# Kernel tuning notes

Measured on AMD Instinct MI355X. Metric: run time of the kernel, lower is better.

Reference implementation:

```python
import jax, jax.numpy as jnp
import numpy as np

EPS = 1e-12  # F.normalize default eps


def setup_inputs() -> dict:
    key = jax.random.key(0)
    x = jax.random.normal(key, (4, 64, 8192, 1), dtype=jnp.float32)
    return {"x": x, "k": 9, "dilation": 1}


def reference(x, k, dilation):
    # x: (B, D, N, 1)
    B, D, N, _ = x.shape
    kk = k * dilation
    # F.normalize(x, p=2, dim=1)
    norm = jnp.linalg.norm(x, axis=1, keepdims=True)
    xn = x / jnp.maximum(norm, EPS)
    # -> (B, N, D)
    pts = jnp.squeeze(xn, -1).transpose(0, 2, 1)
    # pairwise euclidean distance (cdist p=2)
    sq = jnp.sum(pts * pts, axis=-1)  # (B, N)
    d2 = sq[:, :, None] + sq[:, None, :] - 2.0 * jnp.einsum("bnd,bmd->bnm", pts, pts)
    dist = jnp.sqrt(jnp.maximum(d2, 0.0))  # (B, N, N)
    # torch.topk(-dist, k): k smallest distances
    _, nn_idx = jax.lax.top_k(-dist, kk)  # (B, N, kk)
    center_idx = jnp.broadcast_to(jnp.arange(N, dtype=nn_idx.dtype)[None, :, None], (B, N, kk))
    edge_index = jnp.stack([nn_idx, center_idx], axis=0)  # (2, B, N, kk)
    return edge_index[:, :, :, ::dilation]
```

## Files before the change

kernel.cpp:

```cpp
#include <hip/hip_runtime.h>

#define BB 4
#define DD 64
#define NN 8192
#define KK 9


typedef __attribute__((ext_vector_type(8))) _Float16 f16x8;
typedef __attribute__((ext_vector_type(16))) float f32x16;
typedef __attribute__((ext_vector_type(2))) _Float16 h2;
struct H2x4 { h2 a, b, c, d; };

__device__ __forceinline__ uint4 pack8(const unsigned* w) {
    return make_uint4(w[0] | (w[1] << 16), w[2] | (w[3] << 16),
                      w[4] | (w[5] << 16), w[6] | (w[7] << 16));
}

__device__ __forceinline__ float min3f(float a, float b, float c) {
    return fminf(fminf(a, b), c);
}

__device__ __forceinline__ float dot2acc(h2 g, h2 r, float acc) {
#if __has_builtin(__builtin_amdgcn_fdot2)
    return __builtin_amdgcn_fdot2(g, r, acc, false);
#else
    acc = fmaf((float)g[0], (float)r[0], acc);
    return fmaf((float)g[1], (float)r[1], acc);
#endif
}

__device__ __forceinline__ int s_to_j(int g, int s4) {
    int T = ((g >> 6) << 5) + (((g >> 5) & 1) << 4) + (g & 15);
    return T * 32 + ((s4 >> 2) << 3) + (((g >> 4) & 1) << 2) + (s4 & 3);
}

__global__ __launch_bounds__(256) void knorm2_kernel(const float* __restrict__ x,
                                                     float* __restrict__ xnT,
                                                     float* __restrict__ sq,
                                                     unsigned short* __restrict__ Phi,
                                                     unsigned short* __restrict__ Shi) {
    int t = blockIdx.x * 256 + threadIdx.x;
    int b = t >> 13;
    int n = t & (NN - 1);
    const float* xb = x + (size_t)b * DD * NN + n;
    float v[DD];
    float ss = 0.0f;
#pragma unroll
    for (int d = 0; d < DD; ++d) {
        v[d] = xb[(size_t)d * NN];
        ss = fmaf(v[d], v[d], ss);
    }
    float inv = 1.0f / fmaxf(sqrtf(ss), 1e-12f);
    float s2 = 0.0f;
#pragma unroll
    for (int d = 0; d < DD; ++d) {
        v[d] *= inv;
        s2 = fmaf(v[d], v[d], s2);
    }
    sq[t] = s2;
    float4* o4 = reinterpret_cast<float4*>(xnT + (size_t)t * DD);
#pragma unroll
    for (int d = 0; d < DD; d += 4) o4[d >> 2] = make_float4(v[d], v[d+1], v[d+2], v[d+3]);

    size_t base = (size_t)t * DD;
#pragma unroll
    for (int d0 = 0; d0 < DD; d0 += 8) {
        unsigned ph[8], sh[8];
#pragma unroll
        for (int e = 0; e < 8; ++e) {
            float f = v[d0 + e];
            _Float16 hp = (_Float16)f;
            _Float16 hs = (_Float16)(-2.0f * f);
            ph[e] = (unsigned)__builtin_bit_cast(unsigned short, hp);
            sh[e] = (unsigned)__builtin_bit_cast(unsigned short, hs);
        }
        *reinterpret_cast<uint4*>(Phi + base + d0) = pack8(ph);
        *reinterpret_cast<uint4*>(Shi + base + d0) = pack8(sh);
    }
}

__global__ __launch_bounds__(256, 4) void kmin_kernel(const unsigned short* __restrict__ Shi,
                                                      const unsigned short* __restrict__ Phi,
                                                      unsigned short* __restrict__ minbuf16) {
    __shared__ float stage[4][64][33];
    const int lane = threadIdx.x & 63;
    const int wave = threadIdx.x >> 6;
    const int l31 = lane & 31;
    const int half = lane >> 5;
    const int i0 = blockIdx.x * 256 + wave * 64;
    const int b = i0 >> 13;
    const int jloc0 = blockIdx.y * (NN / 8);

    f16x8 Bh0[4], Bh1[4];
    {
        const size_t ib0 = (size_t)(i0 + l31) * DD + half * 8;
        const size_t ib1 = (size_t)(i0 + 32 + l31) * DD + half * 8;
#pragma unroll
        for (int kc = 0; kc < 4; ++kc) {
            Bh0[kc] = *reinterpret_cast<const f16x8*>(Phi + ib0 + kc * 16);
            Bh1[kc] = *reinterpret_cast<const f16x8*>(Phi + ib1 + kc * 16);
        }
    }
    const size_t ja0 = ((size_t)b * NN + jloc0 + l31) * DD + half * 8;

    f16x8 A0[4], A1[4];
#pragma unroll
    for (int kc = 0; kc < 4; ++kc)
        A0[kc] = *reinterpret_cast<const f16x8*>(Shi + ja0 + kc * 16);

#pragma unroll 2
    for (int u2 = 0; u2 < 16; ++u2) {
        const int t0 = u2 * 2;
        {
            const size_t ja = ja0 + (size_t)(t0 + 1) * 32 * DD;
#pragma unroll
            for (int kc = 0; kc < 4; ++kc)
                A1[kc] = *reinterpret_cast<const f16x8*>(Shi + ja + kc * 16);
        }
        {
            f32x16 c0 = {}, c1 = {};
#pragma unroll
            for (int kc = 0; kc < 4; ++kc)
                c0 = __builtin_amdgcn_mfma_f32_32x32x16_f16(A0[kc], Bh0[kc], c0, 0, 0, 0);
#pragma unroll
            for (int kc = 0; kc < 4; ++kc)
                c1 = __builtin_amdgcn_mfma_f32_32x32x16_f16(A0[kc], Bh1[kc], c1, 0, 0, 0);
            const int col = half * 16 + (t0 & 15);
            {
                float q0 = min3f(c0[0], c0[1], c0[2]);
                float q1 = min3f(c0[3], c0[4], c0[5]);
                float q2 = min3f(c0[6], c0[7], c0[8]);
                float q3 = min3f(c0[9], c0[10], c0[11]);
                float q4 = min3f(c0[12], c0[13], c0[14]);
                stage[wave][l31][col] = fminf(min3f(q0, q1, q2), min3f(q3, q4, c0[15]));
            }
            {
                float q0 = min3f(c1[0], c1[1], c1[2]);
                float q1 = min3f(c1[3], c1[4], c1[5]);
                float q2 = min3f(c1[6], c1[7], c1[8]);
                float q3 = min3f(c1[9], c1[10], c1[11]);
                float q4 = min3f(c1[12], c1[13], c1[14]);
                stage[wave][32 + l31][col] = fminf(min3f(q0, q1, q2), min3f(q3, q4, c1[15]));
            }
        }
        if (u2 < 15) {
            const size_t ja = ja0 + (size_t)(t0 + 2) * 32 * DD;
#pragma unroll
            for (int kc = 0; kc < 4; ++kc)
                A0[kc] = *reinterpret_cast<const f16x8*>(Shi + ja + kc * 16);
        }
        {
            f32x16 c0 = {}, c1 = {};
#pragma unroll
            for (int kc = 0; kc < 4; ++kc)
                c0 = __builtin_amdgcn_mfma_f32_32x32x16_f16(A1[kc], Bh0[kc], c0, 0, 0, 0);
#pragma unroll
            for (int kc = 0; kc < 4; ++kc)
                c1 = __builtin_amdgcn_mfma_f32_32x32x16_f16(A1[kc], Bh1[kc], c1, 0, 0, 0);
            const int col = half * 16 + ((t0 + 1) & 15);
            {
                float q0 = min3f(c0[0], c0[1], c0[2]);
                float q1 = min3f(c0[3], c0[4], c0[5]);
                float q2 = min3f(c0[6], c0[7], c0[8]);
                float q3 = min3f(c0[9], c0[10], c0[11]);
                float q4 = min3f(c0[12], c0[13], c0[14]);
                stage[wave][l31][col] = fminf(min3f(q0, q1, q2), min3f(q3, q4, c0[15]));
            }
            {
                float q0 = min3f(c1[0], c1[1], c1[2]);
                float q1 = min3f(c1[3], c1[4], c1[5]);
                float q2 = min3f(c1[6], c1[7], c1[8]);
                float q3 = min3f(c1[9], c1[10], c1[11]);
                float q4 = min3f(c1[12], c1[13], c1[14]);
                stage[wave][32 + l31][col] = fminf(min3f(q0, q1, q2), min3f(q3, q4, c1[15]));
            }
        }
        if ((t0 & 15) == 14) {
            const int fph = t0 >> 4;
            unsigned short* dst0 = minbuf16 + (size_t)blockIdx.y * 64 + fph * 32;
#pragma unroll
            for (int it = 0; it < 4; ++it) {
                int idx = it * 64 + lane;
                int r = idx >> 2;
                int p = idx & 3;
                const float* s = &stage[wave][r][p * 8];
                unsigned w[8];
#pragma unroll
                for (int e = 0; e < 8; ++e)
                    w[e] = (unsigned)__builtin_bit_cast(unsigned short, (_Float16)s[e]);
                *reinterpret_cast<uint4*>(dst0 + (size_t)(i0 + r) * 512 + p * 8) = pack8(w);
            }
        }
    }
}

__global__ __launch_bounds__(256) void ksel_kernel(const float* __restrict__ xnT,
                                                   const float* __restrict__ sq,
                                                   const unsigned short* __restrict__ minbuf16,
                                                   const unsigned short* __restrict__ Phi,
                                                   int* __restrict__ out) {
    __shared__ unsigned short glist[4][2][40];
    __shared__ unsigned short jlist[4][2][64];
    const int lane = threadIdx.x & 63;
    const int wave = threadIdx.x >> 6;
    const int tA = __builtin_amdgcn_readfirstlane(blockIdx.x * 8 + wave * 2);
    const int tB = tA + 1;
    const int b = tA >> 13;
    const int nA = tA & (NN - 1);
    const int nB = tB & (NN - 1);

    float gmA[8], gmB[8];
    {
        uint4 a = *reinterpret_cast<const uint4*>(minbuf16 + (size_t)tA * 512 + lane * 8);
        uint4 c = *reinterpret_cast<const uint4*>(minbuf16 + (size_t)tB * 512 + lane * 8);
        unsigned wa[4] = {a.x, a.y, a.z, a.w};
        unsigned wb[4] = {c.x, c.y, c.z, c.w};
#pragma unroll
        for (int q4 = 0; q4 < 4; ++q4) {
            gmA[q4*2+0] = (float)__builtin_bit_cast(_Float16, (unsigned short)(wa[q4] & 0xFFFFu));
            gmA[q4*2+1] = (float)__builtin_bit_cast(_Float16, (unsigned short)(wa[q4] >> 16));
            gmB[q4*2+0] = (float)__builtin_bit_cast(_Float16, (unsigned short)(wb[q4] & 0xFFFFu));
            gmB[q4*2+1] = (float)__builtin_bit_cast(_Float16, (unsigned short)(wb[q4] >> 16));
        }
    }

    float svA = fminf(min3f(gmA[0], gmA[1], gmA[2]),
                      fminf(min3f(gmA[3], gmA[4], gmA[5]), fminf(gmA[6], gmA[7])));
    float svB = fminf(min3f(gmB[0], gmB[1], gmB[2]),
                      fminf(min3f(gmB[3], gmB[4], gmB[5]), fminf(gmB[6], gmB[7])));
#pragma unroll
    for (int k = 2; k <= 64; k <<= 1) {
#pragma unroll
        for (int jj = k >> 1; jj >= 1; jj >>= 1) {
            float oA = __shfl_xor(svA, jj);
            float oB = __shfl_xor(svB, jj);
            bool keepMin = (((lane & jj) == 0) == ((lane & k) == 0));
            svA = keepMin ? fminf(svA, oA) : fmaxf(svA, oA);
            svB = keepMin ? fminf(svB, oB) : fmaxf(svB, oB);
        }
    }
    const float th9pA = __shfl(svA, 8);
    const float th9pB = __shfl(svB, 8);
    const float thetaA  = th9pA + 8e-3f,  thetaB  = th9pB + 8e-3f;
    const float kappa1A = th9pA + 7.5e-3f, kappa1B = th9pB + 7.5e-3f;

    int cntA = 0, cntB = 0;
    unsigned short* glA = &glist[wave][0][0];
    unsigned short* glB = &glist[wave][1][0];
#pragma unroll
    for (int q = 0; q < 8; ++q) {
        bool cA = gmA[q] <= thetaA;
        unsigned long long mA = __ballot(cA);
        int pA = cntA + __popcll(mA & ((1ULL << lane) - 1ULL));
        if (cA && pA < 40) glA[pA] = (unsigned short)(lane * 8 + q);
        cntA += (int)__popcll(mA);
        bool cB = gmB[q] <= thetaB;
        unsigned long long mB = __ballot(cB);
        int pB = cntB + __popcll(mB & ((1ULL << lane) - 1ULL));
        if (cB && pB < 40) glB[pB] = (unsigned short)(lane * 8 + q);
        cntB += (int)__popcll(mB);
    }

    const unsigned short* __restrict__ Pb = Phi + ((size_t)b * NN) * DD;
    H2x4 arhA[8], arhB[8];
    {
        const f16x8* prA = reinterpret_cast<const f16x8*>(Phi + (size_t)tA * DD);
        const f16x8* prB = reinterpret_cast<const f16x8*>(Phi + (size_t)tB * DD);
#pragma unroll
        for (int c8 = 0; c8 < 8; ++c8) {
            arhA[c8] = __builtin_bit_cast(H2x4, prA[c8]);
            arhB[c8] = __builtin_bit_cast(H2x4, prB[c8]);
        }
    }

    const bool ovfA = (cntA > 40), ovfB = (cntB > 40);
    const int totalA = ovfA ? NN : cntA * 16;
    const int totalB = ovfB ? NN : cntB * 16;
    const int nItA = (totalA + 63) >> 6, nItB = (totalB + 63) >> 6;
    const int nIt = nItA > nItB ? nItA : nItB;
    int S1A = 0, S1B = 0;
    unsigned short* jlA = &jlist[wave][0][0];
    unsigned short* jlB = &jlist[wave][1][0];
#pragma unroll 1
    for (int m = 0; m < nIt; ++m) {
        const int idx = m * 64 + lane;
        const bool actA = idx < totalA;
        const bool actB = idx < totalB;
        float m2A = __uint_as_float(0x7f800000u);
        float m2B = __uint_as_float(0x7f800000u);
        int jA = 0, jB = 0;
        if (actA) {
            jA = ovfA ? idx : s_to_j((int)glA[idx >> 4], idx & 15);
            const f16x8* p8 = reinterpret_cast<const f16x8*>(Pb + (size_t)jA * DD);
            float a0 = 0.0f, a1 = 0.0f, a2 = 0.0f, a3 = 0.0f;
#pragma unroll
            for (int c8 = 0; c8 < 8; ++c8) {
                H2x4 g2 = __builtin_bit_cast(H2x4, p8[c8]);
                a0 = dot2acc(g2.a, arhA[c8].a, a0);
                a1 = dot2acc(g2.b, arhA[c8].b, a1);
                a2 = dot2acc(g2.c, arhA[c8].c, a2);
                a3 = dot2acc(g2.d, arhA[c8].d, a3);
            }
            m2A = -2.0f * ((a0 + a1) + (a2 + a3));
        }
        if (actB) {
            jB = ovfB ? idx : s_to_j((int)glB[idx >> 4], idx & 15);
            const f16x8* p8 = reinterpret_cast<const f16x8*>(Pb + (size_t)jB * DD);
            float a0 = 0.0f, a1 = 0.0f, a2 = 0.0f, a3 = 0.0f;
#pragma unroll
            for (int c8 = 0; c8 < 8; ++c8) {
                H2x4 g2 = __builtin_bit_cast(H2x4, p8[c8]);
                a0 = dot2acc(g2.a, arhB[c8].a, a0);
                a1 = dot2acc(g2.b, arhB[c8].b, a1);
                a2 = dot2acc(g2.c, arhB[c8].c, a2);
                a3 = dot2acc(g2.d, arhB[c8].d, a3);
            }
            m2B = -2.0f * ((a0 + a1) + (a2 + a3));
        }
        bool passA = actA && (m2A <= kappa1A);
        unsigned long long mA = __ballot(passA);
        int pA = S1A + __popcll(mA & ((1ULL << lane) - 1ULL));
        if (passA && pA < 64) jlA[pA] = (unsigned short)jA;
        S1A += (int)__popcll(mA);
        bool passB = actB && (m2B <= kappa1B);
        unsigned long long mB = __ballot(passB);
        int pB = S1B + __popcll(mB & ((1ULL << lane) - 1ULL));
        if (passB && pB < 64) jlB[pB] = (unsigned short)jB;
        S1B += (int)__popcll(mB);
    }

    const float* __restrict__ Bb = xnT + (size_t)b * NN * DD;
    const float* __restrict__ sqb = sq + (size_t)b * NN;

    unsigned long long vA = ~0ULL, vB = ~0ULL;
    {
        float4 bufA[4], bufB[4];
        int jA = 0, jB = 0;
        const bool hvA = lane < (S1A <= 64 ? S1A : 64);
        const bool hvB = lane < (S1B <= 64 ? S1B : 64);
        if (hvA) {
            jA = (int)jlA[lane];
            const float4* bc4 = reinterpret_cast<const float4*>(Bb + (size_t)jA * DD);
#pragma unroll
            for (int p = 0; p < 4; ++p) bufA[p] = bc4[p * 4];
        }
        if (hvB) {
            jB = (int)jlB[lane];
            const float4* bc4 = reinterpret_cast<const float4*>(Bb + (size_t)jB * DD);
#pragma unroll
            for (int p = 0; p < 4; ++p) bufB[p] = bc4[p * 4];
        }
        {
            float ar[DD];
            const float4* a4 = reinterpret_cast<const float4*>(xnT + (size_t)tA * DD);
#pragma unroll
            for (int d = 0; d < DD; d += 4) {
                float4 f = a4[d >> 2];
                ar[d] = f.x; ar[d+1] = f.y; ar[d+2] = f.z; ar[d+3] = f.w;
            }
            if (hvA) {
                const float4* bc4 = reinterpret_cast<const float4*>(Bb + (size_t)jA * DD);
                float a0 = 0, a1 = 0, a2 = 0, a3 = 0;
#pragma unroll
                for (int d4 = 0; d4 < 16; ++d4) {
                    float4 f = (d4 % 4 == 0) ? bufA[d4 / 4] : bc4[d4];
                    a0 = fmaf(ar[4*d4+0], f.x, a0);
                    a1 = fmaf(ar[4*d4+1], f.y, a1);
                    a2 = fmaf(ar[4*d4+2], f.z, a2);
                    a3 = fmaf(ar[4*d4+3], f.w, a3);
                }
                float dot = (a0 + a1) + (a2 + a3);
                float key = fmaf(-2.0f, dot, sqb[jA]);
                unsigned ub = __float_as_uint(key);
                ub ^= (0x80000000u | (unsigned)((int)ub >> 31));
                vA = ((unsigned long long)ub << 32) | (unsigned)jA;
            }
        }
        {
            float ar[DD];
            const float4* a4 = reinterpret_cast<const float4*>(xnT + (size_t)tB * DD);
#pragma unroll
            for (int d = 0; d < DD; d += 4) {
                float4 f = a4[d >> 2];
                ar[d] = f.x; ar[d+1] = f.y; ar[d+2] = f.z; ar[d+3] = f.w;
            }
            if (hvB) {
                const float4* bc4 = reinterpret_cast<const float4*>(Bb + (size_t)jB * DD);
                float a0 = 0, a1 = 0, a2 = 0, a3 = 0;
#pragma unroll
                for (int d4 = 0; d4 < 16; ++d4) {
                    float4 f = (d4 % 4 == 0) ? bufB[d4 / 4] : bc4[d4];
                    a0 = fmaf(ar[4*d4+0], f.x, a0);
                    a1 = fmaf(ar[4*d4+1], f.y, a1);
                    a2 = fmaf(ar[4*d4+2], f.z, a2);
                    a3 = fmaf(ar[4*d4+3], f.w, a3);
                }
                float dot = (a0 + a1) + (a2 + a3);
                float key = fmaf(-2.0f, dot, sqb[jB]);
                unsigned ub = __float_as_uint(key);
                ub ^= (0x80000000u | (unsigned)((int)ub >> 31));
                vB = ((unsigned long long)ub << 32) | (unsigned)jB;
            }
        }
    }
#pragma unroll
    for (int k = 2; k <= 64; k <<= 1) {
#pragma unroll
        for (int jj = k >> 1; jj >= 1; jj >>= 1) {
            unsigned long long oA = __shfl_xor(vA, jj);
            unsigned long long oB = __shfl_xor(vB, jj);
            bool keepMin = (((lane & jj) == 0) == ((lane & k) == 0));
            {
                bool less = oA < vA;
                unsigned long long mn = less ? oA : vA;
                unsigned long long mx = less ? vA : oA;
                vA = keepMin ? mn : mx;
            }
            {
                bool less = oB < vB;
                unsigned long long mn = less ? oB : vB;
                unsigned long long mx = less ? vB : oB;
                vB = keepMin ? mn : mx;
            }
        }
    }
    unsigned long long koutA = vA, koutB = vB;

    auto exact_kd = [&](int tX, int totalX, bool ovfX,
                        const unsigned short* glX) -> unsigned long long {
        float ar[DD];
        const float4* a4 = reinterpret_cast<const float4*>(xnT + (size_t)tX * DD);
#pragma unroll
        for (int d = 0; d < DD; d += 4) {
            float4 f = a4[d >> 2];
            ar[d] = f.x; ar[d+1] = f.y; ar[d+2] = f.z; ar[d+3] = f.w;
        }
        unsigned long long kd[KK];
#pragma unroll
        for (int m = 0; m < KK; ++m) kd[m] = ~0ULL;
        const int nI = (totalX + 63) >> 6;
#pragma unroll 1
        for (int m = 0; m < nI; ++m) {
            const int idx = m * 64 + lane;
            if (idx >= totalX) continue;
            int j = ovfX ? idx : s_to_j((int)glX[idx >> 4], idx & 15);
            const float4* bc4 = reinterpret_cast<const float4*>(Bb + (size_t)j * DD);
            float a0 = 0, a1 = 0, a2 = 0, a3 = 0;
#pragma unroll
            for (int d4 = 0; d4 < 16; ++d4) {
                float4 f = bc4[d4];
                a0 = fmaf(ar[4*d4+0], f.x, a0);
                a1 = fmaf(ar[4*d4+1], f.y, a1);
                a2 = fmaf(ar[4*d4+2], f.z, a2);
                a3 = fmaf(ar[4*d4+3], f.w, a3);
            }
            float dot = (a0 + a1) + (a2 + a3);
            float key = fmaf(-2.0f, dot, sqb[j]);
            unsigned ub = __float_as_uint(key);
            ub ^= (0x80000000u | (unsigned)((int)ub >> 31));
            unsigned long long cnd = ((unsigned long long)ub << 32) | (unsigned)j;
            if (cnd < kd[KK - 1]) {
#pragma unroll
                for (int m2 = 0; m2 < KK; ++m2) {
                    bool sw = cnd < kd[m2];
                    unsigned long long lo = sw ? cnd : kd[m2];
                    unsigned long long hi = sw ? kd[m2] : cnd;
                    kd[m2] = lo;
                    cnd = hi;
                }
            }
        }
        unsigned long long ko = ~0ULL;
#pragma unroll
        for (int r = 0; r < KK; ++r) {
            unsigned long long c = kd[0];
            unsigned long long wm = c;
#pragma unroll
            for (int d = 1; d < 64; d <<= 1) {
                unsigned long long o = __shfl_xor(wm, d);
                wm = (o < wm) ? o : wm;
            }
            if (lane == r) ko = wm;
            if (c == wm) {
#pragma unroll
                for (int m2 = 0; m2 < KK - 1; ++m2) kd[m2] = kd[m2 + 1];
                kd[KK - 1] = ~0ULL;
            }
        }
        return ko;
    };
    if (S1A > 64) koutA = exact_kd(tA, totalA, ovfA, glA);
    if (S1B > 64) koutB = exact_kd(tB, totalB, ovfB, glB);

    if (lane < KK) {
        out[(size_t)tA * KK + lane] = (int)(koutA & 0xFFFFFFFFULL);
        out[(size_t)BB * NN * KK + (size_t)tA * KK + lane] = nA;
        out[(size_t)tB * KK + lane] = (int)(koutB & 0xFFFFFFFFULL);
        out[(size_t)BB * NN * KK + (size_t)tB * KK + lane] = nB;
    }
}

__global__ __launch_bounds__(256) void knorm_kernel(const float* __restrict__ x,
                                                    float* __restrict__ xnT,
                                                    float* __restrict__ sq) {
    int t = blockIdx.x * 256 + threadIdx.x;
    int b = t >> 13;
    int n = t & (NN - 1);
    const float* xb = x + (size_t)b * DD * NN + n;
    float v[DD];
    float ss = 0.0f;
#pragma unroll
    for (int d = 0; d < DD; ++d) {
        v[d] = xb[(size_t)d * NN];
        ss = fmaf(v[d], v[d], ss);
    }
    float norm = sqrtf(ss);
    float inv = 1.0f / fmaxf(norm, 1e-12f);
    float s2 = 0.0f;
#pragma unroll
    for (int d = 0; d < DD; ++d) {
        float xv = v[d] * inv;
        v[d] = xv;
        s2 = fmaf(xv, xv, s2);
    }
    float4* o4 = reinterpret_cast<float4*>(xnT + (size_t)t * DD);
#pragma unroll
    for (int d = 0; d < DD; d += 4) {
        o4[d >> 2] = make_float4(v[d], v[d + 1], v[d + 2], v[d + 3]);
    }
    sq[t] = s2;
}

template <int S>
__global__ __launch_bounds__(256, 2) void kdist_kernel(const float* __restrict__ xnT,
                                                       const float* __restrict__ sq,
                                                       unsigned long long* __restrict__ cand) {
    const int rb = blockIdx.x;
    const int b = rb >> 5;
    const int nbase = (rb & 31) * 256;
    const int n = nbase + threadIdx.x;
    const int s = blockIdx.y;
    const int jcount = NN / S;
    const int j0 = s * jcount;
    const int j1 = j0 + jcount;

    const float* __restrict__ Bb = xnT + ((size_t)b * NN) * DD;
    const float* __restrict__ sqb = sq + (size_t)b * NN;

    float ar[DD];
    {
        const float4* a4 = reinterpret_cast<const float4*>(Bb + (size_t)n * DD);
#pragma unroll
        for (int d = 0; d < DD; d += 4) {
            float4 f = a4[d >> 2];
            ar[d] = f.x; ar[d + 1] = f.y; ar[d + 2] = f.z; ar[d + 3] = f.w;
        }
    }
#pragma unroll
    for (int d = 0; d < DD; ++d) {
        asm volatile("" : "+v"(ar[d]));
    }

    unsigned long long kd[KK];
#pragma unroll
    for (int m = 0; m < KK; ++m) kd[m] = ~0ULL;

#pragma unroll 2
    for (int j = j0; j < j1; ++j) {
        const float4* bc4 = reinterpret_cast<const float4*>(Bb + (size_t)j * DD);
        float a0 = 0.0f, a1 = 0.0f, a2 = 0.0f, a3 = 0.0f;
#pragma unroll
        for (int d4 = 0; d4 < DD / 4; ++d4) {
            float4 f = bc4[d4];
            a0 = fmaf(ar[4 * d4 + 0], f.x, a0);
            a1 = fmaf(ar[4 * d4 + 1], f.y, a1);
            a2 = fmaf(ar[4 * d4 + 2], f.z, a2);
            a3 = fmaf(ar[4 * d4 + 3], f.w, a3);
        }
        float dot = (a0 + a1) + (a2 + a3);
        float key = fmaf(-2.0f, dot, sqb[j]);
        unsigned int ub = __float_as_uint(key);
        ub ^= (0x80000000u | (unsigned int)((int)ub >> 31));
        unsigned long long cnd = ((unsigned long long)ub << 32) | (unsigned int)j;
        if (cnd < kd[KK - 1]) {
#pragma unroll
            for (int m = 0; m < KK; ++m) {
                bool sw = cnd < kd[m];
                unsigned long long lo = sw ? cnd : kd[m];
                unsigned long long hi = sw ? kd[m] : cnd;
                kd[m] = lo;
                cnd = hi;
            }
        }
    }

    unsigned long long* outc = cand + ((size_t)(b * NN + n) * S + s) * KK;
#pragma unroll
    for (int m = 0; m < KK; ++m) outc[m] = kd[m];
}

template <int S>
__global__ __launch_bounds__(256) void kmerge_kernel(const unsigned long long* __restrict__ cand,
                                                     int* __restrict__ out) {
    int t = blockIdx.x * 256 + threadIdx.x;
    const unsigned long long* c = cand + (size_t)t * (S * KK);
    unsigned long long kd[KK];
#pragma unroll
    for (int m = 0; m < KK; ++m) kd[m] = ~0ULL;
#pragma unroll
    for (int q = 0; q < S * KK; ++q) {
        unsigned long long cnd = c[q];
        if (cnd < kd[KK - 1]) {
#pragma unroll
            for (int m = 0; m < KK; ++m) {
                bool sw = cnd < kd[m];
                unsigned long long lo = sw ? cnd : kd[m];
                unsigned long long hi = sw ? kd[m] : cnd;
                kd[m] = lo;
                cnd = hi;
            }
        }
    }
    int n = t & (NN - 1);
    int* out0 = out + (size_t)t * KK;
    int* out1 = out + (size_t)BB * NN * KK + (size_t)t * KK;
#pragma unroll
    for (int m = 0; m < KK; ++m) {
        out0[m] = (int)(kd[m] & 0xFFFFFFFFULL);
        out1[m] = n;
    }
}

extern "C" void kernel_launch(void* const* d_in, const int* in_sizes, int n_in,
                              void* d_out, int out_size, void* d_ws, size_t ws_size,
                              hipStream_t stream) {
    const float* x = (const float*)d_in[0];
    int* out = (int*)d_out;
    char* ws = (char*)d_ws;

    constexpr size_t XNT_B = (size_t)BB * NN * DD * 4;
    constexpr size_t SQ_B  = (size_t)BB * NN * 4;
    float* xnT = (float*)ws;
    float* sq  = (float*)(ws + XNT_B);

    constexpr size_t BF_B  = (size_t)BB * NN * DD * 2;
    constexpr size_t OFF_PHI = XNT_B + SQ_B;
    constexpr size_t OFF_PLO = OFF_PHI + BF_B;
    constexpr size_t OFF_SHI = OFF_PLO + BF_B;
    constexpr size_t OFF_SLO = OFF_SHI + BF_B;
    constexpr size_t OFF_MIN = OFF_SLO + BF_B;
    constexpr size_t MIN_B   = (size_t)512 * BB * NN * 4;
    constexpr size_t NEED_NEW = OFF_MIN + MIN_B;

    if (ws_size >= NEED_NEW) {
        unsigned short* Phi = (unsigned short*)(ws + OFF_PHI);
        unsigned short* Shi = (unsigned short*)(ws + OFF_SHI);
        unsigned short* minbuf16 = (unsigned short*)(ws + OFF_MIN);

        knorm2_kernel<<<dim3(BB * NN / 256), dim3(256), 0, stream>>>(x, xnT, sq, Phi, Shi);
        kmin_kernel<<<dim3(BB * NN / 256, 8), dim3(256), 0, stream>>>(Shi, Phi, minbuf16);
        ksel_kernel<<<dim3(BB * NN / 8), dim3(256), 0, stream>>>(xnT, sq, minbuf16, Phi, out);
        return;
    }

    unsigned long long* cand = (unsigned long long*)(ws + XNT_B + SQ_B);
    const size_t base = XNT_B + SQ_B;
    const size_t need8 = base + (size_t)BB * NN * 8 * KK * 8;

    knorm_kernel<<<dim3(BB * NN / 256), dim3(256), 0, stream>>>(x, xnT, sq);
    if (ws_size >= need8) {
        kdist_kernel<8><<<dim3(BB * NN / 256, 8), dim3(256), 0, stream>>>(xnT, sq, cand);
        kmerge_kernel<8><<<dim3(BB * NN / 256), dim3(256), 0, stream>>>(cand, out);
    } else {
        kdist_kernel<4><<<dim3(BB * NN / 256, 4), dim3(256), 0, stream>>>(xnT, sq, cand);
        kmerge_kernel<4><<<dim3(BB * NN / 256), dim3(256), 0, stream>>>(cand, out);
    }
}
```

Baseline: 243.2 us.

## Stage shared j-tiles in LDS with double buffering and halve per-block j range

The min-distance kernel now loads each 32-row tile of candidate points once per block into a swizzled, double-buffered LDS array shared by all four waves, instead of every wave loading it from global memory. The j-range per block is halved (grid y doubled from 8 to 16), staging is stored as fp16, and each block writes its 32 group-minima once at the end. The s_to_j index mapping is updated to match the new group layout. This cuts redundant global/L2 reads of Shi and increases parallelism, at the cost of a __syncthreads per tile and reloading the B fragments twice as often across blocks.

```diff
diff --git a/kernel.cpp b/kernel.cpp
--- a/kernel.cpp
+++ b/kernel.cpp
@@ -30,8 +30,8 @@
 }
 
 __device__ __forceinline__ int s_to_j(int g, int s4) {
-    int T = ((g >> 6) << 5) + (((g >> 5) & 1) << 4) + (g & 15);
-    return T * 32 + ((s4 >> 2) << 3) + (((g >> 4) & 1) << 2) + (s4 & 3);
+    int T = ((g >> 5) << 4) + (g & 15);
+    return (T << 5) + ((s4 >> 2) << 3) + (((g >> 4) & 1) << 2) + (s4 & 3);
 }
 
 __global__ __launch_bounds__(256) void knorm2_kernel(const float* __restrict__ x,
@@ -82,14 +82,17 @@
 __global__ __launch_bounds__(256, 4) void kmin_kernel(const unsigned short* __restrict__ Shi,
                                                       const unsigned short* __restrict__ Phi,
                                                       unsigned short* __restrict__ minbuf16) {
-    __shared__ float stage[4][64][33];
-    const int lane = threadIdx.x & 63;
-    const int wave = threadIdx.x >> 6;
+    __shared__ unsigned short Ast[2][2048];
+    __shared__ unsigned short stage[4][64][34];
+    const int tid = threadIdx.x;
+    const int lane = tid & 63;
+    const int wave = tid >> 6;
     const int l31 = lane & 31;
     const int half = lane >> 5;
     const int i0 = blockIdx.x * 256 + wave * 64;
-    const int b = i0 >> 13;
-    const int jloc0 = blockIdx.y * (NN / 8);
+    const int b = blockIdx.x >> 5;
+    const int jloc0 = blockIdx.y * 512;
+    const size_t jrow0 = (size_t)b * NN + jloc0;
 
     f16x8 Bh0[4], Bh1[4];
     {
@@ -101,96 +104,74 @@
             Bh1[kc] = *reinterpret_cast<const f16x8*>(Phi + ib1 + kc * 16);
         }
     }
-    const size_t ja0 = ((size_t)b * NN + jloc0 + l31) * DD + half * 8;
-
-    f16x8 A0[4], A1[4];
-#pragma unroll
-    for (int kc = 0; kc < 4; ++kc)
-        A0[kc] = *reinterpret_cast<const f16x8*>(Shi + ja0 + kc * 16);
-
-#pragma unroll 2
-    for (int u2 = 0; u2 < 16; ++u2) {
-        const int t0 = u2 * 2;
+
+    const int srow = tid >> 3;
+    const int sp = tid & 7;
+    const unsigned soff = (unsigned)(srow * 64 + ((sp * 8) ^ ((srow & 7) << 3)));
+    const size_t gbase = (jrow0 + srow) * DD + sp * 8;
+
+    {
+        uint4 g = *reinterpret_cast<const uint4*>(Shi + gbase);
+        *reinterpret_cast<uint4*>(&Ast[0][soff]) = g;
+    }
+    __syncthreads();
+
+    int cur = 0;
+#pragma unroll 1
+    for (int t = 0; t < 16; ++t) {
+        uint4 gnext;
+        const bool hasNext = (t + 1) < 16;
+        if (hasNext)
+            gnext = *reinterpret_cast<const uint4*>(Shi + gbase + (size_t)(t + 1) * 32 * DD);
+
+        f16x8 Ah[4];
+#pragma unroll
+        for (int kc = 0; kc < 4; ++kc) {
+            unsigned off = (unsigned)(l31 * 64 + ((half * 8 + kc * 16) ^ ((l31 & 7) << 3)));
+            Ah[kc] = *reinterpret_cast<const f16x8*>(&Ast[cur][off]);
+        }
+        f32x16 c0 = {}, c1 = {};
+#pragma unroll
+        for (int kc = 0; kc < 4; ++kc)
+            c0 = __builtin_amdgcn_mfma_f32_32x32x16_f16(Ah[kc], Bh0[kc], c0, 0, 0, 0);
+#pragma unroll
+        for (int kc = 0; kc < 4; ++kc)
+            c1 = __builtin_amdgcn_mfma_f32_32x32x16_f16(Ah[kc], Bh1[kc], c1, 0, 0, 0);
+        const int col = half * 16 + t;
         {
-            const size_t ja = ja0 + (size_t)(t0 + 1) * 32 * DD;
-#pragma unroll
-            for (int kc = 0; kc < 4; ++kc)
-                A1[kc] = *reinterpret_cast<const f16x8*>(Shi + ja + kc * 16);
+            float q0 = min3f(c0[0], c0[1], c0[2]);
+            float q1 = min3f(c0[3], c0[4], c0[5]);
+            float q2 = min3f(c0[6], c0[7], c0[8]);
+            float q3 = min3f(c0[9], c0[10], c0[11]);
+            float q4 = min3f(c0[12], c0[13], c0[14]);
+            float mv = fminf(min3f(q0, q1, q2), min3f(q3, q4, c0[15]));
+            stage[wave][l31][col] = (unsigned short)__builtin_bit_cast(unsigned short, (_Float16)mv);
         }
         {
-            f32x16 c0 = {}, c1 = {};
-#pragma unroll
-            for (int kc = 0; kc < 4; ++kc)
-                c0 = __builtin_amdgcn_mfma_f32_32x32x16_f16(A0[kc], Bh0[kc], c0, 0, 0, 0);
-#pragma unroll
-            for (int kc = 0; kc < 4; ++kc)
-                c1 = __builtin_amdgcn_mfma_f32_32x32x16_f16(A0[kc], Bh1[kc], c1, 0, 0, 0);
-            const int col = half * 16 + (t0 & 15);
-            {
-                float q0 = min3f(c0[0], c0[1], c0[2]);
-                float q1 = min3f(c0[3], c0[4], c0[5]);
-                float q2 = min3f(c0[6], c0[7], c0[8]);
-                float q3 = min3f(c0[9], c0[10], c0[11]);
-                float q4 = min3f(c0[12], c0[13], c0[14]);
-                stage[wave][l31][col] = fminf(min3f(q0, q1, q2), min3f(q3, q4, c0[15]));
-            }
-            {
-                float q0 = min3f(c1[0], c1[1], c1[2]);
-                float q1 = min3f(c1[3], c1[4], c1[5]);
-                float q2 = min3f(c1[6], c1[7], c1[8]);
-                float q3 = min3f(c1[9], c1[10], c1[11]);
-                float q4 = min3f(c1[12], c1[13], c1[14]);
-                stage[wave][32 + l31][col] = fminf(min3f(q0, q1, q2), min3f(q3, q4, c1[15]));
-            }
-        }
-        if (u2 < 15) {
-            const size_t ja = ja0 + (size_t)(t0 + 2) * 32 * DD;
-#pragma unroll
-            for (int kc = 0; kc < 4; ++kc)
-                A0[kc] = *reinterpret_cast<const f16x8*>(Shi + ja + kc * 16);
-        }
-        {
-            f32x16 c0 = {}, c1 = {};
-#pragma unroll
-            for (int kc = 0; kc < 4; ++kc)
-                c0 = __builtin_amdgcn_mfma_f32_32x32x16_f16(A1[kc], Bh0[kc], c0, 0, 0, 0);
-#pragma unroll
-            for (int kc = 0; kc < 4; ++kc)
-                c1 = __builtin_amdgcn_mfma_f32_32x32x16_f16(A1[kc], Bh1[kc], c1, 0, 0, 0);
-            const int col = half * 16 + ((t0 + 1) & 15);
-            {
-                float q0 = min3f(c0[0], c0[1], c0[2]);
-                float q1 = min3f(c0[3], c0[4], c0[5]);
-                float q2 = min3f(c0[6], c0[7], c0[8]);
-                float q3 = min3f(c0[9], c0[10], c0[11]);
-                float q4 = min3f(c0[12], c0[13], c0[14]);
-                stage[wave][l31][col] = fminf(min3f(q0, q1, q2), min3f(q3, q4, c0[15]));
-            }
-            {
-                float q0 = min3f(c1[0], c1[1], c1[2]);
-                float q1 = min3f(c1[3], c1[4], c1[5]);
-                float q2 = min3f(c1[6], c1[7], c1[8]);
-                float q3 = min3f(c1[9], c1[10], c1[11]);
-                float q4 = min3f(c1[12], c1[13], c1[14]);
-                stage[wave][32 + l31][col] = fminf(min3f(q0, q1, q2), min3f(q3, q4, c1[15]));
-            }
-        }
-        if ((t0 & 15) == 14) {
-            const int fph = t0 >> 4;
-            unsigned short* dst0 = minbuf16 + (size_t)blockIdx.y * 64 + fph * 32;
-#pragma unroll
-            for (int it = 0; it < 4; ++it) {
-                int idx = it * 64 + lane;
-                int r = idx >> 2;
-                int p = idx & 3;
-                const float* s = &stage[wave][r][p * 8];
-                unsigned w[8];
-#pragma unroll
-                for (int e = 0; e < 8; ++e)
-                    w[e] = (unsigned)__builtin_bit_cast(unsigned short, (_Float16)s[e]);
-                *reinterpret_cast<uint4*>(dst0 + (size_t)(i0 + r) * 512 + p * 8) = pack8(w);
-            }
-        }
+            float q0 = min3f(c1[0], c1[1], c1[2]);
+            float q1 = min3f(c1[3], c1[4], c1[5]);
+            float q2 = min3f(c1[6], c1[7], c1[8]);
+            float q3 = min3f(c1[9], c1[10], c1[11]);
+            float q4 = min3f(c1[12], c1[13], c1[14]);
+            float mv = fminf(min3f(q0, q1, q2), min3f(q3, q4, c1[15]));
+            stage[wave][32 + l31][col] = (unsigned short)__builtin_bit_cast(unsigned short, (_Float16)mv);
+        }
+
+        if (hasNext)
+            *reinterpret_cast<uint4*>(&Ast[cur ^ 1][soff]) = gnext;
+        __syncthreads();
+        cur ^= 1;
+    }
+
+    unsigned short* dst0 = minbuf16 + (size_t)blockIdx.y * 32;
+#pragma unroll
+    for (int it = 0; it < 4; ++it) {
+        int idx = it * 64 + lane;
+        int r = idx >> 2;
+        int p = idx & 3;
+        const unsigned* s32 = reinterpret_cast<const unsigned*>(&stage[wave][r][p * 8]);
+        uint4 vv = make_uint4(s32[0], s32[1], s32[2], s32[3]);
+        *reinterpret_cast<uint4*>(dst0 + (size_t)(i0 + r) * 512 + p * 8) = vv;
     }
 }
 
@@ -658,7 +639,7 @@
         unsigned short* minbuf16 = (unsigned short*)(ws + OFF_MIN);
 
         knorm2_kernel<<<dim3(BB * NN / 256), dim3(256), 0, stream>>>(x, xnT, sq, Phi, Shi);
-        kmin_kernel<<<dim3(BB * NN / 256, 8), dim3(256), 0, stream>>>(Shi, Phi, minbuf16);
+        kmin_kernel<<<dim3(BB * NN / 256, 16), dim3(256), 0, stream>>>(Shi, Phi, minbuf16);
         ksel_kernel<<<dim3(BB * NN / 8), dim3(256), 0, stream>>>(xnT, sq, minbuf16, Phi, out);
         return;
     }
```

Result: faster. 213.7 us (-12.1%).
